# Performance work log

Measured on AMD Instinct MI355X. Metric: run time of the kernel, lower is better.

The kernel has to match this reference:

```python
import jax, jax.numpy as jnp
import numpy as np

# Static architecture sizes (see shape_source)
B, H, W, NCH = 64, 64, 64, 3
K = 2                     # kernel at every stage
D = 20                    # bond_dim == virtual_dim
OUT = 10                  # output_dim
P1 = (H // K) * (W // K)          # 1024 patches, stage 1
P2 = P1 // (K * K)                # 256 patches, stage 2
P3 = P2 // (K * K)                # 64 patches, stage 3
FP = 2 * K * K                    # feature_dim per stage = 2*ker^2 = 8
FF = 2 * D                        # feature_dim of final MPS = 2*virtual_dim


def _unfold(x, k):
    # torch: x.unfold(2,k,k).unfold(3,k,k).reshape(b, k*k, -1, C)
    b, C, Hh, Ww = x.shape
    v = x.reshape(b, C, Hh // k, k, Ww // k, k).transpose(0, 1, 2, 4, 3, 5)
    return v.reshape(b, k * k, -1, C)   # [b, k^2, P, C] (raw reshape, faithful)


def _batchnorm(y, g, bb, eps=1e-5):
    # BatchNorm1d(C) on [b, C, L], training mode (batch stats), affine
    mu = jnp.mean(y, axis=(0, 2), keepdims=True)
    var = jnp.var(y, axis=(0, 2), keepdims=True)
    return g[None, :, None] * (y - mu) * jax.lax.rsqrt(var + eps) + bb[None, :, None]


def _mps(x, cores, label, alpha, omega):
    # Batched tensor-train contraction over independent per-patch MPS modules.
    # x:     [b, Fraw, P, S]  (S sites per MPS, P independent MPS modules)
    # cores: [P, S, 2*Fraw, D, D], label: [O, D, D], alpha/omega: [D]
    phi = jnp.concatenate([x, 1.0 - x], axis=1)              # [b, F, P, S]
    M = jnp.einsum('bfps,psfij->spbij', phi, cores)          # per-site transfer mats
    def step(c, m):
        return jnp.einsum('pbij,pbjk->pbik', c, m), None
    eye = jnp.broadcast_to(jnp.eye(cores.shape[-1], dtype=x.dtype), M.shape[1:])
    tot, _ = jax.lax.scan(step, eye, M)                      # [P, b, D, D]
    return jnp.einsum('i,pbij,ojk,k->bpo', alpha, tot, label, omega)  # [b, P, O]


def _cores(key, P, S, F):
    # near-identity init; sum_f phi_f = Fraw = F/2, so scale eye by 2/F
    return (jnp.eye(D, dtype=jnp.float32) * (2.0 / F)
            + 0.01 * jax.random.normal(key, (P, S, F, D, D), jnp.float32))


def setup_inputs() -> dict:
    ks = jax.random.split(jax.random.key(0), 12)
    one, zero = jnp.ones((D,), jnp.float32), jnp.zeros
    return {
        'x': jax.random.normal(ks[0], (B, NCH, H, W), jnp.float32),
        'cores1': _cores(ks[1], P1, NCH, FP),
        'label1': 0.1 * jax.random.normal(ks[2], (D, D, D), jnp.float32),
        'alpha1': one, 'omega1': one,
        'g1': jnp.ones((P1,), jnp.float32), 'b1': zero((P1,), jnp.float32),
        'cores2': _cores(ks[3], P2, D, FP),
        'label2': 0.1 * jax.random.normal(ks[4], (D, D, D), jnp.float32),
        'alpha2': one, 'omega2': one,
        'g2': jnp.ones((P2,), jnp.float32), 'b2': zero((P2,), jnp.float32),
        'cores3': _cores(ks[5], P3, D, FP),
        'label3': 0.1 * jax.random.normal(ks[6], (D, D, D), jnp.float32),
        'alpha3': one, 'omega3': one,
        'g3': jnp.ones((P3,), jnp.float32), 'b3': zero((P3,), jnp.float32),
        'coresF': _cores(ks[7], 1, P3, FF),
        'labelF': 0.1 * jax.random.normal(ks[8], (OUT, D, D), jnp.float32),
        'alphaF': one, 'omegaF': one,
    }


def reference(x, cores1, label1, alpha1, omega1, g1, b1,
              cores2, label2, alpha2, omega2, g2, b2,
              cores3, label3, alpha3, omega3, g3, b3,
              coresF, labelF, alphaF, omegaF):
    b = x.shape[0]
    u = _unfold(x, K)                              # [b, 4, P1, 3]
    y = _mps(u, cores1, label1, alpha1, omega1)    # [b, P1, D]
    y = _batchnorm(y, g1, b1).reshape(b, D, H // K, W // K)   # raw view, faithful
    u = _unfold(y, K)                              # [b, 4, P2, D]
    y = _mps(u, cores2, label2, alpha2, omega2)    # [b, P2, D]
    y = _batchnorm(y, g2, b2).reshape(b, D, H // (K * K), W // (K * K))
    u = _unfold(y, K)                              # [b, 4, P3, D]
    y = _mps(u, cores3, label3, alpha3, omega3)    # [b, P3, D]
    y = _batchnorm(y, g3, b3)
    y = jnp.transpose(y, (0, 2, 1))                # [b, D, P3]
    out = _mps(y[:, :, None, :], coresF, labelF, alphaF, omegaF)[:, 0, :]
    return out                                     # [b, OUT]
```

## Files before the change

### kernel.cpp

```cpp
#include <hip/hip_runtime.h>
#include <hip/hip_bf16.h>

typedef __attribute__((ext_vector_type(4))) float f32x4;
typedef __attribute__((ext_vector_type(8))) short s16x8;

static __device__ __forceinline__ short f2bf(float x) {
  __hip_bfloat16 h = __float2bfloat16(x);
  return *reinterpret_cast<short*>(&h);
}

template<int STAGE>
__global__ __launch_bounds__(256)
void k_mps(const float* __restrict__ xsrc, const float* __restrict__ ysrc,
           const float* __restrict__ cores, const float* __restrict__ alpha,
           const float* __restrict__ label, const float* __restrict__ omega,
           const float* __restrict__ gam, const float* __restrict__ bet,
           float* __restrict__ yout) {
  constexpr int S = (STAGE == 1) ? 3 : 20;
  __shared__ __align__(16) float u4[S][64][4];
  __shared__ __align__(16) short Cl[2][32][168];
  __shared__ __align__(16) float vls[64][36];
  __shared__ float Lw_l[400];
  __shared__ float redA[4], redB[4], stats[2];

  const int p = blockIdx.x, t = threadIdx.x;
  const int b = t & 63, q = t >> 6;
  const int m = b & 15, quad = b >> 4;
  const int bl = q * 16 + m;

  const bool two = (t < 144);
  const float* cbase = cores + (size_t)p * S * 3200;

  float p0A[8], p0B[8], p1A[8], p1B[8];
#pragma unroll
  for (int g = 0; g < 8; ++g) p0A[g] = cbase[g * 400 + t];
  if (two) {
#pragma unroll
    for (int g = 0; g < 8; ++g) p0B[g] = cbase[g * 400 + 256 + t];
  }

  for (int e = t; e < 400; e += 256) {
    int o = e / 20, j = e % 20;
    float a = 0.f;
#pragma unroll
    for (int k = 0; k < 20; ++k) a = fmaf(label[o * 400 + j * 20 + k], omega[k], a);
    Lw_l[e] = a;
  }

  {
    int* cz = (int*)&Cl[0][0][0];
    for (int i = t; i < 5376; i += 256) cz[i] = 0;
    for (int i = t; i < 64 * 36; i += 256) {
      int col = i % 36;
      vls[i / 36][col] = (col < 20) ? alpha[col] : 0.f;
    }
  }

  for (int k = 0; k < S; ++k) {
    float val;
    if (STAGE == 1) {
      int L = q * 3072 + p * 3 + k;
      int c = L >> 12, r = L & 4095;
      int hh = 2 * (r >> 7) + ((r >> 1) & 1);
      int ww = 2 * ((r >> 2) & 31) + (r & 1);
      val = xsrc[(b * 3 + c) * 4096 + hh * 64 + ww];
    } else if (STAGE == 2) {
      int L = q * 5120 + p * 20 + k;
      int c = L >> 10, r = L & 1023;
      int f = c * 1024 + (2 * (r >> 6) + ((r >> 1) & 1)) * 32
                        + (2 * ((r >> 2) & 15) + (r & 1));
      val = ysrc[f * 64 + b];
    } else {
      int L = q * 1280 + p * 20 + k;
      int c = L >> 8, r = L & 255;
      int f = c * 256 + (2 * (r >> 5) + ((r >> 1) & 1)) * 16
                       + (2 * ((r >> 2) & 7) + (r & 1));
      val = ysrc[f * 64 + b];
    }
    u4[k][b][q] = val;
  }

  auto writeC = [&](int buf, int e, const float* r) {
    int i = e / 20, j = e % 20;
    Cl[buf][j][      i] = f2bf(r[0] - r[4]);
    Cl[buf][j][ 32 + i] = f2bf(r[1] - r[5]);
    Cl[buf][j][ 64 + i] = f2bf(r[2] - r[6]);
    Cl[buf][j][ 96 + i] = f2bf(r[3] - r[7]);
    float cs = r[4] + r[5] + r[6] + r[7];
    if (i == j) cs -= 1.f;
    Cl[buf][j][128 + i] = f2bf(cs);
  };
  auto loadSite = [&](int s, float (&rA)[8], float (&rB)[8]) {
    const float* cs = cbase + (size_t)s * 3200;
#pragma unroll
    for (int g = 0; g < 8; ++g) rA[g] = cs[g * 400 + t];
    if (two) {
#pragma unroll
      for (int g = 0; g < 8; ++g) rB[g] = cs[g * 400 + 256 + t];
    }
  };

  writeC(0, t, p0A);
  if (two) writeC(0, t + 256, p0B);
  if (S > 1) loadSite(1, p0A, p0B);
  if (S > 2) loadSite(2, p1A, p1B);
  __syncthreads();

  auto site_step = [&](int s, int cur, float (&rA)[8], float (&rB)[8]) {
    const float4 uu = *(const float4*)&u4[s][bl][0];
    const float4 va = *(const float4*)&vls[bl][quad * 8];
    const float4 vb = *(const float4*)&vls[bl][quad * 8 + 4];
    const float vv[8] = {va.x, va.y, va.z, va.w, vb.x, vb.y, vb.z, vb.w};
    const float um[5] = {uu.x, uu.y, uu.z, uu.w, 1.f};

    f32x4 acc0 = {0.f, 0.f, 0.f, 0.f};
    f32x4 acc1 = {0.f, 0.f, 0.f, 0.f};
#pragma unroll
    for (int kt = 0; kt < 5; ++kt) {
      s16x8 aF;
#pragma unroll
      for (int j2 = 0; j2 < 8; ++j2) aF[j2] = f2bf(vv[j2] * um[kt]);
      const s16x8 bF0 = *(const s16x8*)&Cl[cur][m][kt * 32 + quad * 8];
      const s16x8 bF1 = *(const s16x8*)&Cl[cur][m + 16][kt * 32 + quad * 8];
      acc0 = __builtin_amdgcn_mfma_f32_16x16x32_bf16(aF, bF0, acc0, 0, 0, 0);
      acc1 = __builtin_amdgcn_mfma_f32_16x16x32_bf16(aF, bF1, acc1, 0, 0, 0);
    }

    if (s + 1 < S) {
      writeC(cur ^ 1, t, rA);
      if (two) writeC(cur ^ 1, t + 256, rB);
      if (s + 3 < S) loadSite(s + 3, rA, rB);
    }

#pragma unroll
    for (int r = 0; r < 4; ++r) vls[q * 16 + quad * 4 + r][m] += acc0[r];
    if (m < 4) {
#pragma unroll
      for (int r = 0; r < 4; ++r) vls[q * 16 + quad * 4 + r][m + 16] += acc1[r];
    }
    __syncthreads();
  };

  for (int s = 0; s < S; s += 2) {
    site_step(s, 0, p0A, p0B);
    if (s + 1 < S) site_step(s + 1, 1, p1A, p1B);
  }

  float vf[20];
  {
    const float4 v0 = *(const float4*)&vls[b][0];
    const float4 v1 = *(const float4*)&vls[b][4];
    const float4 v2 = *(const float4*)&vls[b][8];
    const float4 v3 = *(const float4*)&vls[b][12];
    const float4 v4 = *(const float4*)&vls[b][16];
    vf[0]=v0.x; vf[1]=v0.y; vf[2]=v0.z; vf[3]=v0.w;
    vf[4]=v1.x; vf[5]=v1.y; vf[6]=v1.z; vf[7]=v1.w;
    vf[8]=v2.x; vf[9]=v2.y; vf[10]=v2.z; vf[11]=v2.w;
    vf[12]=v3.x; vf[13]=v3.y; vf[14]=v3.z; vf[15]=v3.w;
    vf[16]=v4.x; vf[17]=v4.y; vf[18]=v4.z; vf[19]=v4.w;
  }
  float yo[5];
  float s1 = 0.f, s2 = 0.f;
#pragma unroll
  for (int jj = 0; jj < 5; ++jj) {
    int o = q * 5 + jj;
    float a = 0.f;
#pragma unroll
    for (int j = 0; j < 20; ++j) a = fmaf(vf[j], Lw_l[o * 20 + j], a);
    yo[jj] = a; s1 += a; s2 += a * a;
  }
#pragma unroll
  for (int off = 32; off > 0; off >>= 1) {
    s1 += __shfl_down(s1, off); s2 += __shfl_down(s2, off);
  }
  if (b == 0) { redA[q] = s1; redB[q] = s2; }
  __syncthreads();
  if (t == 0) {
    float S1 = redA[0] + redA[1] + redA[2] + redA[3];
    float S2 = redB[0] + redB[1] + redB[2] + redB[3];
    float mu = S1 * (1.f / 1280.f);
    float var = S2 * (1.f / 1280.f) - mu * mu;
    if (var < 0.f) var = 0.f;
    stats[0] = mu; stats[1] = var;
  }
  __syncthreads();
  float mu = stats[0], var = stats[1];
  float scale = gam[p] / sqrtf(var + 1e-5f);
  float shift = bet[p] - mu * scale;
#pragma unroll
  for (int jj = 0; jj < 5; ++jj) {
    int o = q * 5 + jj;
    yout[(p * 20 + o) * 64 + b] = fmaf(yo[jj], scale, shift);
  }
}

__global__ __launch_bounds__(256)
void k_f1(const float* __restrict__ y3n, const float* __restrict__ coresF,
          float* __restrict__ PP) {
  const int bid = blockIdx.x;
  const int b = bid >> 3, c = bid & 7;
  const int t = threadIdx.x;
  __shared__ float ybuf[8][20];
  __shared__ float M[400];
  __shared__ float Pb[2][400];
  if (t < 160) ybuf[t / 20][t % 20] = y3n[(c * 160 + t) * 64 + b];
  __syncthreads();
  int cur = 0;
  for (int s = 0; s < 8; ++s) {
    const float* cf = coresF + (size_t)(c * 8 + s) * 16000;
    for (int e = t; e < 400; e += 256) {
      float m = 0.f;
#pragma unroll
      for (int g = 0; g < 20; ++g) {
        float lo = cf[g * 400 + e];
        float hi = cf[(g + 20) * 400 + e];
        m += fmaf(ybuf[s][g], lo - hi, hi);
      }
      M[e] = m;
    }
    __syncthreads();
    if (s == 0) {
      for (int e = t; e < 400; e += 256) Pb[0][e] = M[e];
    } else {
      for (int e = t; e < 400; e += 256) {
        int i = e / 20, j = e % 20;
        float a = 0.f;
#pragma unroll
        for (int k = 0; k < 20; ++k)
          a = fmaf(Pb[cur][i * 20 + k], M[k * 20 + j], a);
        Pb[cur ^ 1][e] = a;
      }
      cur ^= 1;
    }
    __syncthreads();
  }
  for (int e = t; e < 400; e += 256) PP[(size_t)bid * 400 + e] = Pb[cur][e];
}

__global__ __launch_bounds__(256)
void k_f2(const float* __restrict__ PP, const float* __restrict__ alphaF,
          const float* __restrict__ labelF, const float* __restrict__ omegaF,
          float* __restrict__ out) {
  const int b = blockIdx.x, t = threadIdx.x;
  __shared__ float Pb[2][400];
  __shared__ float M[400];
  __shared__ float va[20];
  __shared__ float LwF_l[200];
  if (t < 200) {
    int o = t / 20, j = t % 20;
    float a = 0.f;
#pragma unroll
    for (int k = 0; k < 20; ++k) a = fmaf(labelF[o * 400 + j * 20 + k], omegaF[k], a);
    LwF_l[t] = a;
  }
  for (int e = t; e < 400; e += 256) Pb[0][e] = PP[(size_t)b * 3200 + e];
  int cur = 0;
  for (int c = 1; c < 8; ++c) {
    for (int e = t; e < 400; e += 256) M[e] = PP[(size_t)b * 3200 + c * 400 + e];
    __syncthreads();
    for (int e = t; e < 400; e += 256) {
      int i = e / 20, j = e % 20;
      float a = 0.f;
#pragma unroll
      for (int k = 0; k < 20; ++k) a = fmaf(Pb[cur][i * 20 + k], M[k * 20 + j], a);
      Pb[cur ^ 1][e] = a;
    }
    cur ^= 1;
    __syncthreads();
  }
  if (t < 20) {
    float a = 0.f;
#pragma unroll
    for (int i = 0; i < 20; ++i) a = fmaf(alphaF[i], Pb[cur][i * 20 + t], a);
    va[t] = a;
  }
  __syncthreads();
  if (t < 10) {
    float a = 0.f;
#pragma unroll
    for (int j = 0; j < 20; ++j) a = fmaf(va[j], LwF_l[t * 20 + j], a);
    out[b * 10 + t] = a;
  }
}

extern "C" void kernel_launch(void* const* d_in, const int* in_sizes, int n_in,
                              void* d_out, int out_size, void* d_ws, size_t ws_size,
                              hipStream_t stream) {
  const float* x      = (const float*)d_in[0];
  const float* cores1 = (const float*)d_in[1];
  const float* label1 = (const float*)d_in[2];
  const float* alpha1 = (const float*)d_in[3];
  const float* omega1 = (const float*)d_in[4];
  const float* g1     = (const float*)d_in[5];
  const float* b1     = (const float*)d_in[6];
  const float* cores2 = (const float*)d_in[7];
  const float* label2 = (const float*)d_in[8];
  const float* alpha2 = (const float*)d_in[9];
  const float* omega2 = (const float*)d_in[10];
  const float* g2     = (const float*)d_in[11];
  const float* b2     = (const float*)d_in[12];
  const float* cores3 = (const float*)d_in[13];
  const float* label3 = (const float*)d_in[14];
  const float* alpha3 = (const float*)d_in[15];
  const float* omega3 = (const float*)d_in[16];
  const float* g3     = (const float*)d_in[17];
  const float* b3     = (const float*)d_in[18];
  const float* coresF = (const float*)d_in[19];
  const float* labelF = (const float*)d_in[20];
  const float* alphaF = (const float*)d_in[21];
  const float* omegaF = (const float*)d_in[22];

  float* ws  = (float*)d_ws;
  float* yn1 = ws;
  float* yn2 = yn1 + 1310720;
  float* yn3 = yn2 + 327680;
  float* PP  = yn3 + 81920;
  float* out = (float*)d_out;

  k_mps<1><<<1024, 256, 0, stream>>>(x, nullptr, cores1, alpha1, label1, omega1, g1, b1, yn1);
  k_mps<2><<<256, 256, 0, stream>>>(nullptr, yn1, cores2, alpha2, label2, omega2, g2, b2, yn2);
  k_mps<3><<<64, 256, 0, stream>>>(nullptr, yn2, cores3, alpha3, label3, omega3, g3, b3, yn3);
  k_f1<<<512, 256, 0, stream>>>(yn3, coresF, PP);
  k_f2<<<64, 256, 0, stream>>>(PP, alphaF, labelF, omegaF, out);
}
```

Before: 255.1 us.

## Build final-stage transfer matrices once per site, chain sequentially per batch

```diff
diff --git a/kernel.cpp b/kernel.cpp
--- a/kernel.cpp
+++ b/kernel.cpp
@@ -194,75 +194,74 @@
   }
 }
 
+
 __global__ __launch_bounds__(256)
-void k_f1(const float* __restrict__ y3n, const float* __restrict__ coresF,
-          float* __restrict__ PP) {
-  const int bid = blockIdx.x;
-  const int b = bid >> 3, c = bid & 7;
+void k_mbuild(const float* __restrict__ yn3, const float* __restrict__ coresF,
+              float* __restrict__ Mmat) {
+  __shared__ float ybn[64][20];
+  const int s = blockIdx.x >> 2, bq = blockIdx.x & 3;
   const int t = threadIdx.x;
-  __shared__ float ybuf[8][20];
-  __shared__ float M[400];
-  __shared__ float Pb[2][400];
-  if (t < 160) ybuf[t / 20][t % 20] = y3n[(c * 160 + t) * 64 + b];
-  __syncthreads();
-  int cur = 0;
-  for (int s = 0; s < 8; ++s) {
-    const float* cf = coresF + (size_t)(c * 8 + s) * 16000;
-    for (int e = t; e < 400; e += 256) {
-      float m = 0.f;
-#pragma unroll
-      for (int g = 0; g < 20; ++g) {
-        float lo = cf[g * 400 + e];
-        float hi = cf[(g + 20) * 400 + e];
-        m += fmaf(ybuf[s][g], lo - hi, hi);
-      }
-      M[e] = m;
-    }
-    __syncthreads();
-    if (s == 0) {
-      for (int e = t; e < 400; e += 256) Pb[0][e] = M[e];
-    } else {
-      for (int e = t; e < 400; e += 256) {
-        int i = e / 20, j = e % 20;
-        float a = 0.f;
-#pragma unroll
-        for (int k = 0; k < 20; ++k)
-          a = fmaf(Pb[cur][i * 20 + k], M[k * 20 + j], a);
-        Pb[cur ^ 1][e] = a;
-      }
-      cur ^= 1;
-    }
-    __syncthreads();
-  }
-  for (int e = t; e < 400; e += 256) PP[(size_t)bid * 400 + e] = Pb[cur][e];
+  for (int i = t; i < 1280; i += 256) ybn[i & 63][i >> 6] = yn3[(size_t)s * 1280 + i];
+  __syncthreads();
+  const float* cfp = coresF + (size_t)s * 16000;
+  for (int e = t; e < 400; e += 256) {
+    float dlt[20]; float hsum = 0.f;
+#pragma unroll
+    for (int g = 0; g < 20; ++g) {
+      float lo = cfp[g * 400 + e], hi = cfp[(g + 20) * 400 + e];
+      dlt[g] = lo - hi; hsum += hi;
+    }
+    for (int bb = bq * 16; bb < bq * 16 + 16; ++bb) {
+      const float4* yb = (const float4*)ybn[bb];
+      float yy[20];
+      *(float4*)&yy[0]  = yb[0]; *(float4*)&yy[4]  = yb[1];
+      *(float4*)&yy[8]  = yb[2]; *(float4*)&yy[12] = yb[3];
+      *(float4*)&yy[16] = yb[4];
+      float a = hsum;
+#pragma unroll
+      for (int g = 0; g < 20; ++g) a = fmaf(yy[g], dlt[g], a);
+      Mmat[((size_t)s * 64 + bb) * 400 + e] = a;
+    }
+  }
 }
 
 __global__ __launch_bounds__(256)
-void k_f2(const float* __restrict__ PP, const float* __restrict__ alphaF,
-          const float* __restrict__ labelF, const float* __restrict__ omegaF,
-          float* __restrict__ out) {
+void k_chain(const float* __restrict__ Mmat, const float* __restrict__ alphaF,
+             const float* __restrict__ labelF, const float* __restrict__ omegaF,
+             float* __restrict__ out) {
   const int b = blockIdx.x, t = threadIdx.x;
   __shared__ float Pb[2][400];
-  __shared__ float M[400];
+  __shared__ float Mb[2][400];
+  __shared__ float LwF[200];
   __shared__ float va[20];
-  __shared__ float LwF_l[200];
+
   if (t < 200) {
     int o = t / 20, j = t % 20;
     float a = 0.f;
 #pragma unroll
     for (int k = 0; k < 20; ++k) a = fmaf(labelF[o * 400 + j * 20 + k], omegaF[k], a);
-    LwF_l[t] = a;
-  }
-  for (int e = t; e < 400; e += 256) Pb[0][e] = PP[(size_t)b * 3200 + e];
+    LwF[t] = a;
+  }
+  for (int e = t; e < 400; e += 256) Pb[0][e] = Mmat[(size_t)b * 400 + e];
+  float r0 = Mmat[(size_t)(64 + b) * 400 + t];
+  float r1 = (t < 144) ? Mmat[(size_t)(64 + b) * 400 + 256 + t] : 0.f;
+  __syncthreads();
+
   int cur = 0;
-  for (int c = 1; c < 8; ++c) {
-    for (int e = t; e < 400; e += 256) M[e] = PP[(size_t)b * 3200 + c * 400 + e];
+  for (int s = 1; s < 64; ++s) {
+    Mb[s & 1][t] = r0;
+    if (t < 144) Mb[s & 1][256 + t] = r1;
     __syncthreads();
+    if (s + 1 < 64) {
+      r0 = Mmat[(size_t)((s + 1) * 64 + b) * 400 + t];
+      if (t < 144) r1 = Mmat[(size_t)((s + 1) * 64 + b) * 400 + 256 + t];
+    }
     for (int e = t; e < 400; e += 256) {
-      int i = e / 20, j = e % 20;
+      int i = e / 20, j = e - (e / 20) * 20;
       float a = 0.f;
 #pragma unroll
-      for (int k = 0; k < 20; ++k) a = fmaf(Pb[cur][i * 20 + k], M[k * 20 + j], a);
+      for (int k = 0; k < 20; ++k)
+        a = fmaf(Pb[cur][i * 20 + k], Mb[s & 1][k * 20 + j], a);
       Pb[cur ^ 1][e] = a;
     }
     cur ^= 1;
@@ -278,7 +277,7 @@
   if (t < 10) {
     float a = 0.f;
 #pragma unroll
-    for (int j = 0; j < 20; ++j) a = fmaf(va[j], LwF_l[t * 20 + j], a);
+    for (int j = 0; j < 20; ++j) a = fmaf(va[j], LwF[t * 20 + j], a);
     out[b * 10 + t] = a;
   }
 }
@@ -310,16 +309,16 @@
   const float* alphaF = (const float*)d_in[21];
   const float* omegaF = (const float*)d_in[22];
 
-  float* ws  = (float*)d_ws;
-  float* yn1 = ws;
-  float* yn2 = yn1 + 1310720;
-  float* yn3 = yn2 + 327680;
-  float* PP  = yn3 + 81920;
-  float* out = (float*)d_out;
+  float* ws   = (float*)d_ws;
+  float* yn1  = ws;
+  float* yn2  = yn1 + 1310720;
+  float* yn3  = yn2 + 327680;
+  float* Mmat = yn3 + 81920;
+  float* out  = (float*)d_out;
 
   k_mps<1><<<1024, 256, 0, stream>>>(x, nullptr, cores1, alpha1, label1, omega1, g1, b1, yn1);
   k_mps<2><<<256, 256, 0, stream>>>(nullptr, yn1, cores2, alpha2, label2, omega2, g2, b2, yn2);
   k_mps<3><<<64, 256, 0, stream>>>(nullptr, yn2, cores3, alpha3, label3, omega3, g3, b3, yn3);
-  k_f1<<<512, 256, 0, stream>>>(yn3, coresF, PP);
-  k_f2<<<64, 256, 0, stream>>>(PP, alphaF, labelF, omegaF, out);
-}
+  k_mbuild<<<256, 256, 0, stream>>>(yn3, coresF, Mmat);
+  k_chain<<<64, 256, 0, stream>>>(Mmat, alphaF, labelF, omegaF, out);
+}
```

Result: slower. 282.4 us (+10.7%).
